# Performance work log

Measured on AMD Instinct MI355X. Metric: run time of the kernel, lower is better.

Reference implementation:

```python
import jax, jax.numpy as jnp
import numpy as np
import math

D, H, NQP, NKP = 512, 8, 4, 4
DH = D // H
OUT_DIM = D + H * NKP * 3  # 608


def setup_inputs() -> dict:
    key = jax.random.key(0)
    ks = jax.random.split(key, 12)
    B, L = 2, 1024
    s = jax.random.normal(ks[0], (B, L, D), dtype=jnp.float32)
    R = jax.random.normal(ks[1], (B, L, 3, 3), dtype=jnp.float32)
    tr = jax.random.normal(ks[2], (B, L, 3), dtype=jnp.float32)
    sc = 0.02
    Wq = jax.random.normal(ks[3], (D, D), dtype=jnp.float32) * sc
    Wk = jax.random.normal(ks[4], (D, D), dtype=jnp.float32) * sc
    Wv = jax.random.normal(ks[5], (D, D), dtype=jnp.float32) * sc
    Wqp = jax.random.normal(ks[6], (D, H * NQP * 3), dtype=jnp.float32) * sc
    Wkp = jax.random.normal(ks[7], (D, H * NKP * 3), dtype=jnp.float32) * sc
    Wvp = jax.random.normal(ks[8], (D, H * NKP * 3), dtype=jnp.float32) * sc
    Wo = jax.random.normal(ks[9], (OUT_DIM, D), dtype=jnp.float32) * sc
    bo = jnp.zeros((D,), dtype=jnp.float32)
    gamma = jnp.ones((D,), dtype=jnp.float32)
    beta = jnp.zeros((D,), dtype=jnp.float32)
    w_C = jnp.full((H,), math.log(20.0), dtype=jnp.float32)
    return dict(s=s, R=R, tr=tr, Wq=Wq, Wk=Wk, Wv=Wv, Wqp=Wqp, Wkp=Wkp,
                Wvp=Wvp, Wo=Wo, bo=bo, gamma=gamma, beta=beta, w_C=w_C)


def _layernorm(x, gamma, beta, eps=1e-5):
    mu = jnp.mean(x, axis=-1, keepdims=True)
    var = jnp.var(x, axis=-1, keepdims=True)
    return (x - mu) * jax.lax.rsqrt(var + eps) * gamma + beta


def reference(s, R, tr, Wq, Wk, Wv, Wqp, Wkp, Wvp, Wo, bo, gamma, beta, w_C):
    B, L, _ = s.shape
    # scalar q/k/v: (B, L, H, dh)
    Q = (s @ Wq).reshape(B, L, H, DH)
    K = (s @ Wk).reshape(B, L, H, DH)
    V = (s @ Wv).reshape(B, L, H, DH)
    a_s = jnp.einsum('bihd,bjhd->bhij', Q, K) / math.sqrt(DH)
    # local points: (B, L, H, P, 3)
    Qp = (s @ Wqp).reshape(B, L, H, NQP, 3)
    Kp = (s @ Wkp).reshape(B, L, H, NKP, 3)
    Vp = (s @ Wvp).reshape(B, L, H, NKP, 3)
    tr_e = tr[:, :, None, None, :]
    to_global = lambda p: jnp.einsum('blxy,blhpy->blhpx', R, p) + tr_e
    Qp_g, Kp_g, Vp_g = to_global(Qp), to_global(Kp), to_global(Vp)
    # (B, H, L, P, 3)
    qh = jnp.transpose(Qp_g, (0, 2, 1, 3, 4))
    kh = jnp.transpose(Kp_g, (0, 2, 1, 3, 4))
    diff = qh[:, :, :, None] - kh[:, :, None]          # (B,H,L,L,P,3)
    sq_dist = jnp.sum(diff * diff, axis=(-2, -1))      # (B,H,L,L)
    wc = jax.nn.softplus(w_C)[None, :, None, None]
    attn = jax.nn.softmax(a_s - 0.5 * wc * sq_dist, axis=-1)
    out_s = jnp.einsum('bhij,bjhd->bihd', attn, V).reshape(B, L, D)
    Vp_agg = jnp.einsum('bhij,bjhpc->bihpc', attn, Vp_g)  # (B,L,H,P,3)
    # global -> local: R^T (p - tr)
    Vp_local = jnp.einsum('blyx,blhpy->blhpx', R, Vp_agg - tr_e)
    out_p = Vp_local.reshape(B, L, H * NKP * 3)
    out = jnp.concatenate([out_s, out_p], axis=-1) @ Wo + bo
    return _layernorm(s + out, gamma, beta)
```

## Files before the change

### kernel.cpp

```cpp
#include <hip/hip_runtime.h>
#include <hip/hip_fp16.h>
#include <math.h>

typedef _Float16 f16;
typedef _Float16 f16x8 __attribute__((ext_vector_type(8)));
typedef _Float16 f16x4v __attribute__((ext_vector_type(4)));
typedef float f32x4 __attribute__((ext_vector_type(4)));

#define BATCH   2
#define LSEQ    1024
#define BLTOT   2048
#define DMODEL  512
#define NHEAD   8
#define PDIM    1824
#define AW      96
#define ODIM    608
#define NSPLIT  2

__global__ __launch_bounds__(256)
void prep_kernel(const float* __restrict__ s,
                 const float* __restrict__ Wq, const float* __restrict__ Wk,
                 const float* __restrict__ Wv, const float* __restrict__ Wqp,
                 const float* __restrict__ Wkp, const float* __restrict__ Wvp,
                 const float* __restrict__ Wo,
                 f16* __restrict__ sH, f16* __restrict__ WallT, f16* __restrict__ WoT)
{
    const int blk = blockIdx.x;
    const int t = threadIdx.x;
    __shared__ float tile[32][33];

    if (blk < 1024) {
        const int i = blk * 256 + t;
        float4 v = ((const float4*)s)[i];
        f16x4v o = { (f16)v.x, (f16)v.y, (f16)v.z, (f16)v.w };
        ((f16x4v*)sH)[i] = o;
        return;
    }
    if (blk < 1936) {
        const int idx = blk - 1024;
        const int n0 = (idx % 57) * 32, k0 = (idx / 57) * 32;
        const float* src; int ld, nc0;
        if      (n0 < 512)  { src = Wq;  ld = 512; nc0 = n0; }
        else if (n0 < 1024) { src = Wk;  ld = 512; nc0 = n0 - 512; }
        else if (n0 < 1536) { src = Wv;  ld = 512; nc0 = n0 - 1024; }
        else if (n0 < 1632) { src = Wqp; ld = 96;  nc0 = n0 - 1536; }
        else if (n0 < 1728) { src = Wkp; ld = 96;  nc0 = n0 - 1632; }
        else                { src = Wvp; ld = 96;  nc0 = n0 - 1728; }
#pragma unroll
        for (int i = 0; i < 4; ++i) {
            const int idx2 = t + i * 256;
            const int kl = idx2 >> 5, nl = idx2 & 31;
            tile[kl][nl] = src[(long long)(k0 + kl) * ld + nc0 + nl];
        }
        __syncthreads();
#pragma unroll
        for (int i = 0; i < 4; ++i) {
            const int idx2 = t + i * 256;
            const int nl = idx2 >> 5, kl = idx2 & 31;
            WallT[(long long)(n0 + nl) * 512 + k0 + kl] = (f16)tile[kl][nl];
        }
        return;
    }
    {
        const int idx = blk - 1936;
        const int n0 = (idx % 16) * 32, k0 = (idx / 16) * 32;
#pragma unroll
        for (int i = 0; i < 4; ++i) {
            const int idx2 = t + i * 256;
            const int kl = idx2 >> 5, nl = idx2 & 31;
            tile[kl][nl] = Wo[(long long)(k0 + kl) * 512 + n0 + nl];
        }
        __syncthreads();
#pragma unroll
        for (int i = 0; i < 4; ++i) {
            const int idx2 = t + i * 256;
            const int nl = idx2 >> 5, kl = idx2 & 31;
            WoT[(long long)(n0 + nl) * 608 + k0 + kl] = (f16)tile[kl][nl];
        }
    }
}

template<int BN, bool OUT16>
__global__ __launch_bounds__(256)
void gemm2_kernel(const f16* __restrict__ A, const f16* __restrict__ Bt,
                  void* __restrict__ Cout, int K, int ldc)
{
    constexpr int BCH = (BN * 4 + 255) / 256;
    __shared__ f16 As[2][64][40];
    __shared__ f16 Bs[2][BN][40];
    const int t = threadIdx.x;
    const int w = t >> 6, lane = t & 63, l15 = lane & 15, lhi = lane >> 4;
    const int row0 = blockIdx.y * 64, col0 = blockIdx.x * BN;
    const int ar = t >> 2, ac = t & 3;

    f32x4 acc[BN / 16];
#pragma unroll
    for (int n = 0; n < BN / 16; ++n) acc[n] = (f32x4){0.f, 0.f, 0.f, 0.f};

    const int nsteps = K >> 5;

    f16x8 aR;
    f16x8 bR[BCH];
    aR = *(const f16x8*)&A[(long long)(row0 + ar) * K + ac * 8];
#pragma unroll
    for (int i = 0; i < BCH; ++i) {
        const int cid = t + i * 256;
        if (cid < BN * 4) {
            const int br = cid >> 2, bc = cid & 3;
            bR[i] = *(const f16x8*)&Bt[(long long)(col0 + br) * K + bc * 8];
        }
    }
    *(f16x8*)&As[0][ar][ac * 8] = aR;
#pragma unroll
    for (int i = 0; i < BCH; ++i) {
        const int cid = t + i * 256;
        if (cid < BN * 4) *(f16x8*)&Bs[0][cid >> 2][(cid & 3) * 8] = bR[i];
    }
    __syncthreads();

    for (int st = 0; st < nsteps; ++st) {
        const int cur = st & 1;
        if (st + 1 < nsteps) {
            const int k0 = (st + 1) << 5;
            aR = *(const f16x8*)&A[(long long)(row0 + ar) * K + k0 + ac * 8];
#pragma unroll
            for (int i = 0; i < BCH; ++i) {
                const int cid = t + i * 256;
                if (cid < BN * 4) {
                    const int br = cid >> 2, bc = cid & 3;
                    bR[i] = *(const f16x8*)&Bt[(long long)(col0 + br) * K + k0 + bc * 8];
                }
            }
        }
        f16x8 af = *(const f16x8*)&As[cur][w * 16 + l15][lhi * 8];
        f16x8 bf[BN / 16];
#pragma unroll
        for (int n = 0; n < BN / 16; ++n)
            bf[n] = *(const f16x8*)&Bs[cur][n * 16 + l15][lhi * 8];
#pragma unroll
        for (int n = 0; n < BN / 16; ++n)
            acc[n] = __builtin_amdgcn_mfma_f32_16x16x32_f16(af, bf[n], acc[n], 0, 0, 0);
        if (st + 1 < nsteps) {
            *(f16x8*)&As[cur ^ 1][ar][ac * 8] = aR;
#pragma unroll
            for (int i = 0; i < BCH; ++i) {
                const int cid = t + i * 256;
                if (cid < BN * 4) *(f16x8*)&Bs[cur ^ 1][cid >> 2][(cid & 3) * 8] = bR[i];
            }
        }
        __syncthreads();
    }

    const int row = row0 + w * 16 + lhi * 4;
#pragma unroll
    for (int n = 0; n < BN / 16; ++n) {
        const int col = col0 + n * 16 + l15;
#pragma unroll
        for (int r = 0; r < 4; ++r) {
            if (OUT16) ((f16*)Cout)[(long long)(row + r) * ldc + col] = (f16)acc[n][r];
            else       ((float*)Cout)[(long long)(row + r) * ldc + col] = acc[n][r];
        }
    }
}

__global__ __launch_bounds__(256)
void build_aug2_kernel(const f16* __restrict__ P, const float* __restrict__ Rm,
                       const float* __restrict__ tr, const float* __restrict__ wC,
                       f16* __restrict__ QA, f16* __restrict__ KA,
                       f16* __restrict__ VCT, float* __restrict__ KOFF)
{
    const int l0 = blockIdx.x * 64;
    const int bh = blockIdx.y;
    const int b = bh >> 3, h = bh & 7;
    const int t = threadIdx.x;

    __shared__ float Rl[64][9];
    __shared__ float trl[64][3];
    __shared__ f16 gq[64][12];
    __shared__ f16 gk[64][12];
    __shared__ float k2[64][4];
    __shared__ f16 Vt[96][72];
    __shared__ float wcs;

    const long long blbase = (long long)b * LSEQ + l0;

    for (int i = t; i < 64 * 9; i += 256) Rl[i / 9][i % 9] = Rm[blbase * 9 + i];
    for (int i = t; i < 64 * 3; i += 256) trl[i / 3][i % 3] = tr[blbase * 3 + i];
    if (t == 0) { float x = wC[h]; wcs = log1pf(expf(x)); }
    __syncthreads();
    const float wc = wcs;

    for (int i = t; i < 768; i += 256) {
        const int l = i / 12, pp = i - l * 12;
        const int proj = pp >> 2, p = pp & 3;
        const f16* src = P + (blbase + l) * PDIM + 1536 + proj * 96 + h * 12 + p * 3;
        const float x = (float)src[0], y = (float)src[1], z = (float)src[2];
        const float gx = Rl[l][0]*x + Rl[l][1]*y + Rl[l][2]*z + trl[l][0];
        const float gy = Rl[l][3]*x + Rl[l][4]*y + Rl[l][5]*z + trl[l][1];
        const float gz = Rl[l][6]*x + Rl[l][7]*y + Rl[l][8]*z + trl[l][2];
        if (proj == 0) {
            gq[l][p * 3 + 0] = (f16)(wc * gx);
            gq[l][p * 3 + 1] = (f16)(wc * gy);
            gq[l][p * 3 + 2] = (f16)(wc * gz);
        } else if (proj == 1) {
            gk[l][p * 3 + 0] = (f16)gx;
            gk[l][p * 3 + 1] = (f16)gy;
            gk[l][p * 3 + 2] = (f16)gz;
            k2[l][p] = gx * gx + gy * gy + gz * gz;
        } else {
            Vt[64 + p * 3 + 0][l] = (f16)gx;
            Vt[64 + p * 3 + 1][l] = (f16)gy;
            Vt[64 + p * 3 + 2][l] = (f16)gz;
        }
    }
    for (int i = t; i < 512; i += 256) {
        const int l = i >> 3, ch = i & 7;
        f16x8 v = *(const f16x8*)&P[(blbase + l) * PDIM + 1024 + h * 64 + ch * 8];
#pragma unroll
        for (int j = 0; j < 8; ++j) Vt[ch * 8 + j][l] = v[j];
    }
    for (int i = t; i < 180; i += 256) {
        const int r = 76 + i / 9, ch = i % 9;
        *(f16x8*)&Vt[r][ch * 8] = (f16x8){0,0,0,0,0,0,0,0};
    }
    __syncthreads();

    if (t < 64)
        KOFF[(long long)bh * LSEQ + l0 + t] =
            0.5f * wc * (k2[t][0] + k2[t][1] + k2[t][2] + k2[t][3]);

    for (int i = t; i < 768; i += 256) {
        const int l = i / 12, ch = i - l * 12;
        const long long prow = (blbase + l) * PDIM;
        const long long orow = ((long long)bh * LSEQ + l0 + l) * AW;
        f16x8 q, k;
        if (ch < 8) {
            f16x8 qv = *(const f16x8*)&P[prow + h * 64 + ch * 8];
            f16x8 kv = *(const f16x8*)&P[prow + 512 + h * 64 + ch * 8];
            q = qv * (f16)0.125f;
            k = kv;
        } else if (ch == 8) {
#pragma unroll
            for (int j = 0; j < 8; ++j) { q[j] = gq[l][j]; k[j] = gk[l][j]; }
        } else if (ch == 9) {
#pragma unroll
            for (int j = 0; j < 8; ++j) {
                q[j] = (j < 4) ? gq[l][8 + j] : (f16)0.f;
                k[j] = (j < 4) ? gk[l][8 + j] : (f16)0.f;
            }
        } else {
            q = (f16x8){0,0,0,0,0,0,0,0};
            k = (f16x8){0,0,0,0,0,0,0,0};
        }
        *(f16x8*)&QA[orow + ch * 8] = q;
        *(f16x8*)&KA[orow + ch * 8] = k;
    }
    for (int i = t; i < 768; i += 256) {
        const int c = i >> 3, lg = i & 7;
        *(f16x8*)&VCT[((long long)bh * AW + c) * LSEQ + l0 + lg * 8] =
            *(const f16x8*)&Vt[c][lg * 8];
    }
}

__global__ __launch_bounds__(256, 2)
void attn_kernel(const f16* __restrict__ QA, const f16* __restrict__ KA,
                 const f16* __restrict__ VCT, const float* __restrict__ KOFF,
                 f16* __restrict__ OCp, float2* __restrict__ ML)
{
    const int bh = blockIdx.y;
    const int q0 = blockIdx.x * 64;
    const int z  = blockIdx.z;
    const int t = threadIdx.x;
    const int w = t >> 6, lane = t & 63, l15 = lane & 15, lhi = lane >> 4;

    __shared__ f16 Ks[128][104];
    __shared__ f16 Vs[96][136];
    __shared__ f16 Ps[64][136];

    const f16* qbase = QA + ((long long)bh * LSEQ + q0 + w * 16 + l15) * AW;
    f16x8 qf[3];
#pragma unroll
    for (int ks = 0; ks < 3; ++ks)
        qf[ks] = *(const f16x8*)(qbase + ks * 32 + lhi * 8);

    f32x4 Oacc[6];
#pragma unroll
    for (int nv = 0; nv < 6; ++nv) Oacc[nv] = (f32x4){0.f, 0.f, 0.f, 0.f};
    float M[4], L[4];
#pragma unroll
    for (int r = 0; r < 4; ++r) { M[r] = -1e30f; L[r] = 0.f; }

    const f16* kgbase = KA + (long long)bh * LSEQ * AW;
    const f16* vgbase = VCT + (long long)bh * AW * LSEQ;
    const float* koffb = KOFF + (long long)bh * LSEQ;

    const int kvbeg = z * (LSEQ / NSPLIT);
    const int kvend = kvbeg + LSEQ / NSPLIT;

#pragma unroll
    for (int i = 0; i < 6; ++i) {
        const int cid = t + i * 256;
        const int r = cid / 12, c = cid - r * 12;
        *(f16x8*)&Ks[r][c * 8] = *(const f16x8*)(kgbase + (long long)(kvbeg + r) * AW + c * 8);
    }
#pragma unroll
    for (int i = 0; i < 6; ++i) {
        const int cid = t + i * 256;
        const int r = cid >> 4, c = cid & 15;
        *(f16x8*)&Vs[r][c * 8] = *(const f16x8*)(vgbase + (long long)r * LSEQ + kvbeg + c * 8);
    }
    __syncthreads();

    for (int kv0 = kvbeg; kv0 < kvend; kv0 += 128) {
        const bool more = (kv0 + 128 < kvend);
        f16x8 kpre[6], vpre[6];
        if (more) {
#pragma unroll
            for (int i = 0; i < 6; ++i) {
                const int cid = t + i * 256;
                const int r = cid / 12, c = cid - r * 12;
                kpre[i] = *(const f16x8*)(kgbase + (long long)(kv0 + 128 + r) * AW + c * 8);
            }
#pragma unroll
            for (int i = 0; i < 6; ++i) {
                const int cid = t + i * 256;
                const int r = cid >> 4, c = cid & 15;
                vpre[i] = *(const f16x8*)(vgbase + (long long)r * LSEQ + kv0 + 128 + c * 8);
            }
        }

        f32x4 sc[8];
#pragma unroll
        for (int n = 0; n < 8; ++n) sc[n] = (f32x4){0.f, 0.f, 0.f, 0.f};
        __builtin_amdgcn_s_setprio(1);
#pragma unroll
        for (int n = 0; n < 8; ++n)
#pragma unroll
            for (int ks = 0; ks < 3; ++ks) {
                f16x8 kb = *(const f16x8*)&Ks[n * 16 + l15][ks * 32 + lhi * 8];
                sc[n] = __builtin_amdgcn_mfma_f32_16x16x32_f16(qf[ks], kb, sc[n], 0, 0, 0);
            }
        __builtin_amdgcn_s_setprio(0);
#pragma unroll
        for (int n = 0; n < 8; ++n) {
            const float ko = koffb[kv0 + n * 16 + l15];
#pragma unroll
            for (int r = 0; r < 4; ++r) sc[n][r] -= ko;
        }
        float sscale[4];
#pragma unroll
        for (int r = 0; r < 4; ++r) {
            float mr = sc[0][r];
#pragma unroll
            for (int n = 1; n < 8; ++n) mr = fmaxf(mr, sc[n][r]);
#pragma unroll
            for (int off = 1; off < 16; off <<= 1) mr = fmaxf(mr, __shfl_xor(mr, off));
            const float nm = fmaxf(M[r], mr);
            sscale[r] = __expf(M[r] - nm);
            M[r] = nm;
        }
        float rsum[4] = {0.f, 0.f, 0.f, 0.f};
#pragma unroll
        for (int n = 0; n < 8; ++n)
#pragma unroll
            for (int r = 0; r < 4; ++r) {
                const float p = __expf(sc[n][r] - M[r]);
                sc[n][r] = p;
                rsum[r] += p;
            }
#pragma unroll
        for (int r = 0; r < 4; ++r) {
            float s = rsum[r];
#pragma unroll
            for (int off = 1; off < 16; off <<= 1) s += __shfl_xor(s, off);
            L[r] = L[r] * sscale[r] + s;
        }
#pragma unroll
        for (int nv = 0; nv < 6; ++nv)
#pragma unroll
            for (int r = 0; r < 4; ++r) Oacc[nv][r] *= sscale[r];

#pragma unroll
        for (int n = 0; n < 8; ++n)
#pragma unroll
            for (int r = 0; r < 4; ++r)
                Ps[w * 16 + lhi * 4 + r][n * 16 + l15] = (f16)sc[n][r];

        f16x8 pa[4];
#pragma unroll
        for (int ks = 0; ks < 4; ++ks)
            pa[ks] = *(const f16x8*)&Ps[w * 16 + l15][ks * 32 + lhi * 8];
        __builtin_amdgcn_s_setprio(1);
#pragma unroll
        for (int nv = 0; nv < 6; ++nv)
#pragma unroll
            for (int ks = 0; ks < 4; ++ks) {
                f16x8 vb = *(const f16x8*)&Vs[nv * 16 + l15][ks * 32 + lhi * 8];
                Oacc[nv] = __builtin_amdgcn_mfma_f32_16x16x32_f16(pa[ks], vb, Oacc[nv], 0, 0, 0);
            }
        __builtin_amdgcn_s_setprio(0);
        __syncthreads();

        if (more) {
#pragma unroll
            for (int i = 0; i < 6; ++i) {
                const int cid = t + i * 256;
                const int r = cid / 12, c = cid - r * 12;
                *(f16x8*)&Ks[r][c * 8] = kpre[i];
            }
#pragma unroll
            for (int i = 0; i < 6; ++i) {
                const int cid = t + i * 256;
                const int r = cid >> 4, c = cid & 15;
                *(f16x8*)&Vs[r][c * 8] = vpre[i];
            }
        }
        __syncthreads();
    }

    f16* obase = OCp + (((long long)(z * 16 + bh) * LSEQ) + q0 + w * 16 + lhi * 4) * AW;
#pragma unroll
    for (int nv = 0; nv < 6; ++nv)
#pragma unroll
        for (int r = 0; r < 4; ++r)
            obase[r * AW + nv * 16 + l15] = (f16)Oacc[nv][r];
    if (l15 == 0) {
#pragma unroll
        for (int r = 0; r < 4; ++r)
            ML[(long long)(z * 16 + bh) * LSEQ + q0 + w * 16 + lhi * 4 + r] =
                make_float2(M[r], L[r]);
    }
}

__global__ __launch_bounds__(256)
void combine_concat_kernel(const f16* __restrict__ OCp, const float2* __restrict__ ML,
                           const float* __restrict__ Rm, const float* __restrict__ tr,
                           f16* __restrict__ CC)
{
    const int bl = blockIdx.x;
    const int b = bl >> 10, l = bl & 1023;
    const int t = threadIdx.x;

    __shared__ float w1[8], w2[8];
    __shared__ float o[8][AW];
    __shared__ float Rloc[9], trloc[3];
    if (t < 9) Rloc[t] = Rm[(long long)bl * 9 + t];
    if (t < 3) trloc[t] = tr[(long long)bl * 3 + t];
    if (t < 8) {
        const int bh = b * 8 + t;
        const float2 m1 = ML[(long long)bh * LSEQ + l];
        const float2 m2 = ML[(long long)(16 + bh) * LSEQ + l];
        const float mm = fmaxf(m1.x, m2.x);
        const float e1 = __expf(m1.x - mm), e2 = __expf(m2.x - mm);
        const float inv = 1.0f / (m1.y * e1 + m2.y * e2);
        w1[t] = e1 * inv; w2[t] = e2 * inv;
    }
    __syncthreads();
    for (int idx = t; idx < 8 * AW; idx += 256) {
        const int h = idx / AW, c = idx - h * AW;
        const f16* p1 = OCp + ((long long)(b * 8 + h) * LSEQ + l) * AW;
        const f16* p2 = OCp + ((long long)(16 + b * 8 + h) * LSEQ + l) * AW;
        o[h][c] = (float)p1[c] * w1[h] + (float)p2[c] * w2[h];
    }
    __syncthreads();

    f16* crow = CC + (long long)bl * ODIM;
    for (int c = t; c < DMODEL; c += 256) crow[c] = (f16)o[c >> 6][c & 63];
    if (t < 32) {
        const int h = t >> 2, p = t & 3;
        const float x = o[h][64 + p * 3 + 0] - trloc[0];
        const float y = o[h][64 + p * 3 + 1] - trloc[1];
        const float z = o[h][64 + p * 3 + 2] - trloc[2];
        crow[512 + h * 12 + p * 3 + 0] = (f16)(Rloc[0]*x + Rloc[3]*y + Rloc[6]*z);
        crow[512 + h * 12 + p * 3 + 1] = (f16)(Rloc[1]*x + Rloc[4]*y + Rloc[7]*z);
        crow[512 + h * 12 + p * 3 + 2] = (f16)(Rloc[2]*x + Rloc[5]*y + Rloc[8]*z);
    }
}

__global__ __launch_bounds__(256)
void residual_ln_kernel(const float* __restrict__ s, const float* __restrict__ Y,
                        const float* __restrict__ bo, const float* __restrict__ gamma,
                        const float* __restrict__ beta, float* __restrict__ out)
{
    const int bl = blockIdx.x;
    const int t = threadIdx.x;
    const float* srow = s + (long long)bl * DMODEL;
    const float* yrow = Y + (long long)bl * DMODEL;

    const float v0 = srow[t]       + yrow[t]       + bo[t];
    const float v1 = srow[t + 256] + yrow[t + 256] + bo[t + 256];

    float sum = v0 + v1, sq = v0 * v0 + v1 * v1;
#pragma unroll
    for (int o = 32; o > 0; o >>= 1) {
        sum += __shfl_xor(sum, o);
        sq  += __shfl_xor(sq,  o);
    }
    __shared__ float rs[4], rq[4];
    const int wid = t >> 6, lane = t & 63;
    if (lane == 0) { rs[wid] = sum; rq[wid] = sq; }
    __syncthreads();
    sum = rs[0] + rs[1] + rs[2] + rs[3];
    sq  = rq[0] + rq[1] + rq[2] + rq[3];

    const float mu  = sum * (1.0f / DMODEL);
    const float var = sq * (1.0f / DMODEL) - mu * mu;
    const float inv = rsqrtf(var + 1e-5f);

    out[(long long)bl * DMODEL + t]       = (v0 - mu) * inv * gamma[t]       + beta[t];
    out[(long long)bl * DMODEL + t + 256] = (v1 - mu) * inv * gamma[t + 256] + beta[t + 256];
}

extern "C" void kernel_launch(void* const* d_in, const int* in_sizes, int n_in,
                              void* d_out, int out_size, void* d_ws, size_t ws_size,
                              hipStream_t stream)
{
    const float* s    = (const float*)d_in[0];
    const float* R    = (const float*)d_in[1];
    const float* tr   = (const float*)d_in[2];
    const float* Wq   = (const float*)d_in[3];
    const float* Wk   = (const float*)d_in[4];
    const float* Wv   = (const float*)d_in[5];
    const float* Wqp  = (const float*)d_in[6];
    const float* Wkp  = (const float*)d_in[7];
    const float* Wvp  = (const float*)d_in[8];
    const float* Wo   = (const float*)d_in[9];
    const float* bo   = (const float*)d_in[10];
    const float* gam  = (const float*)d_in[11];
    const float* bet  = (const float*)d_in[12];
    const float* wC   = (const float*)d_in[13];
    float* out = (float*)d_out;

    f16* sH    = (f16*)d_ws;
    f16* WallT = sH + 1048576;
    f16* WoT   = WallT + 933888;
    f16* P     = WoT + 311296;
    f16* QA    = P + 3735552;
    f16* KA    = QA + 1572864;
    f16* VCT   = KA + 1572864;
    float* KOFF = (float*)(VCT + 1572864);
    f16* OCp    = (f16*)(KOFF + 16384);
    float2* ML  = (float2*)(OCp + 3145728);
    f16* CC     = (f16*)(ML + 32768);
    float* Y    = (float*)(CC + 1245184);

    const dim3 blk(256);

    prep_kernel<<<dim3(2240), blk, 0, stream>>>(s, Wq, Wk, Wv, Wqp, Wkp, Wvp, Wo,
                                                sH, WallT, WoT);

    gemm2_kernel<96, true><<<dim3(19, 32), blk, 0, stream>>>(sH, WallT, P, 512, 1824);

    build_aug2_kernel<<<dim3(16, 16), blk, 0, stream>>>(P, R, tr, wC, QA, KA, VCT, KOFF);

    attn_kernel<<<dim3(16, 16, NSPLIT), blk, 0, stream>>>(QA, KA, VCT, KOFF, OCp, ML);

    combine_concat_kernel<<<dim3(BLTOT), blk, 0, stream>>>(OCp, ML, R, tr, CC);

    gemm2_kernel<64, false><<<dim3(8, 32), blk, 0, stream>>>(CC, WoT, Y, 608, 512);

    residual_ln_kernel<<<dim3(BLTOT), blk, 0, stream>>>(s, Y, bo, gam, bet, out);
}
```

Measured before the change: 72.90 us.

## Fuse projection epilogue into GEMM and split-combine into output GEMM

The QKV/point projection GEMM now writes scaled Q, K, transposed V and rigid-transformed point features straight into the attention input layouts from its epilogue. This removes the intermediate P buffer and the separate build kernel. The split-softmax combine and the global-to-local point rotation move into the A-operand load path of the output-projection GEMM, which removes the CC buffer and the combine kernel. The cost is heavier epilogues with scattered narrow stores, recomputed combine weights for each column tile, and extra global reads of OCp per N-tile.

Result: slower. 88.06 us (+20.8%).

```diff
diff --git a/kernel.cpp b/kernel.cpp
--- a/kernel.cpp
+++ b/kernel.cpp
@@ -12,10 +12,9 @@
 #define BLTOT   2048
 #define DMODEL  512
 #define NHEAD   8
-#define PDIM    1824
 #define AW      96
-#define ODIM    608
 #define NSPLIT  2
+#define OCPSTR  1572864
 
 __global__ __launch_bounds__(256)
 void prep_kernel(const float* __restrict__ s,
@@ -80,185 +79,169 @@
     }
 }
 
-template<int BN, bool OUT16>
+struct SmG { f16 As[2][64][40]; f16 Bs[2][96][40]; };
+struct SmE { float pts[64][96]; float Rl[64][9]; float trl[64][3]; };
+
 __global__ __launch_bounds__(256)
-void gemm2_kernel(const f16* __restrict__ A, const f16* __restrict__ Bt,
-                  void* __restrict__ Cout, int K, int ldc)
+void proj_fused_kernel(const f16* __restrict__ A, const f16* __restrict__ Bt,
+                       const float* __restrict__ Rm, const float* __restrict__ tr,
+                       const float* __restrict__ wC,
+                       f16* __restrict__ QA, f16* __restrict__ KA,
+                       f16* __restrict__ VCT, float* __restrict__ KOFF)
 {
-    constexpr int BCH = (BN * 4 + 255) / 256;
-    __shared__ f16 As[2][64][40];
-    __shared__ f16 Bs[2][BN][40];
+    __shared__ union { SmG g; SmE e; } sm;
     const int t = threadIdx.x;
     const int w = t >> 6, lane = t & 63, l15 = lane & 15, lhi = lane >> 4;
-    const int row0 = blockIdx.y * 64, col0 = blockIdx.x * BN;
+    const int row0 = blockIdx.y * 64, col0 = blockIdx.x * 96;
     const int ar = t >> 2, ac = t & 3;
-
-    f32x4 acc[BN / 16];
-#pragma unroll
-    for (int n = 0; n < BN / 16; ++n) acc[n] = (f32x4){0.f, 0.f, 0.f, 0.f};
-
-    const int nsteps = K >> 5;
-
-    f16x8 aR;
-    f16x8 bR[BCH];
+    const int K = 512;
+
+    f32x4 acc[6];
+#pragma unroll
+    for (int n = 0; n < 6; ++n) acc[n] = (f32x4){0.f, 0.f, 0.f, 0.f};
+
+    f16x8 aR, bR[2];
     aR = *(const f16x8*)&A[(long long)(row0 + ar) * K + ac * 8];
 #pragma unroll
-    for (int i = 0; i < BCH; ++i) {
+    for (int i = 0; i < 2; ++i) {
         const int cid = t + i * 256;
-        if (cid < BN * 4) {
+        if (cid < 384) {
             const int br = cid >> 2, bc = cid & 3;
             bR[i] = *(const f16x8*)&Bt[(long long)(col0 + br) * K + bc * 8];
         }
     }
-    *(f16x8*)&As[0][ar][ac * 8] = aR;
-#pragma unroll
-    for (int i = 0; i < BCH; ++i) {
+    *(f16x8*)&sm.g.As[0][ar][ac * 8] = aR;
+#pragma unroll
+    for (int i = 0; i < 2; ++i) {
         const int cid = t + i * 256;
-        if (cid < BN * 4) *(f16x8*)&Bs[0][cid >> 2][(cid & 3) * 8] = bR[i];
+        if (cid < 384) *(f16x8*)&sm.g.Bs[0][cid >> 2][(cid & 3) * 8] = bR[i];
     }
     __syncthreads();
 
-    for (int st = 0; st < nsteps; ++st) {
+    for (int st = 0; st < 16; ++st) {
         const int cur = st & 1;
-        if (st + 1 < nsteps) {
+        if (st + 1 < 16) {
             const int k0 = (st + 1) << 5;
             aR = *(const f16x8*)&A[(long long)(row0 + ar) * K + k0 + ac * 8];
 #pragma unroll
-            for (int i = 0; i < BCH; ++i) {
+            for (int i = 0; i < 2; ++i) {
                 const int cid = t + i * 256;
-                if (cid < BN * 4) {
+                if (cid < 384) {
                     const int br = cid >> 2, bc = cid & 3;
                     bR[i] = *(const f16x8*)&Bt[(long long)(col0 + br) * K + k0 + bc * 8];
                 }
             }
         }
-        f16x8 af = *(const f16x8*)&As[cur][w * 16 + l15][lhi * 8];
-        f16x8 bf[BN / 16];
-#pragma unroll
-        for (int n = 0; n < BN / 16; ++n)
-            bf[n] = *(const f16x8*)&Bs[cur][n * 16 + l15][lhi * 8];
-#pragma unroll
-        for (int n = 0; n < BN / 16; ++n)
+        f16x8 af = *(const f16x8*)&sm.g.As[cur][w * 16 + l15][lhi * 8];
+        f16x8 bf[6];
+#pragma unroll
+        for (int n = 0; n < 6; ++n)
+            bf[n] = *(const f16x8*)&sm.g.Bs[cur][n * 16 + l15][lhi * 8];
+#pragma unroll
+        for (int n = 0; n < 6; ++n)
             acc[n] = __builtin_amdgcn_mfma_f32_16x16x32_f16(af, bf[n], acc[n], 0, 0, 0);
-        if (st + 1 < nsteps) {
-            *(f16x8*)&As[cur ^ 1][ar][ac * 8] = aR;
-#pragma unroll
-            for (int i = 0; i < BCH; ++i) {
+        if (st + 1 < 16) {
+            *(f16x8*)&sm.g.As[cur ^ 1][ar][ac * 8] = aR;
+#pragma unroll
+            for (int i = 0; i < 2; ++i) {
                 const int cid = t + i * 256;
-                if (cid < BN * 4) *(f16x8*)&Bs[cur ^ 1][cid >> 2][(cid & 3) * 8] = bR[i];
+                if (cid < 384) *(f16x8*)&sm.g.Bs[cur ^ 1][cid >> 2][(cid & 3) * 8] = bR[i];
             }
         }
         __syncthreads();
     }
 
-    const int row = row0 + w * 16 + lhi * 4;
-#pragma unroll
-    for (int n = 0; n < BN / 16; ++n) {
-        const int col = col0 + n * 16 + l15;
-#pragma unroll
-        for (int r = 0; r < 4; ++r) {
-            if (OUT16) ((f16*)Cout)[(long long)(row + r) * ldc + col] = (f16)acc[n][r];
-            else       ((float*)Cout)[(long long)(row + r) * ldc + col] = acc[n][r];
-        }
-    }
-}
-
-__global__ __launch_bounds__(256)
-void build_aug2_kernel(const f16* __restrict__ P, const float* __restrict__ Rm,
-                       const float* __restrict__ tr, const float* __restrict__ wC,
-                       f16* __restrict__ QA, f16* __restrict__ KA,
-                       f16* __restrict__ VCT, float* __restrict__ KOFF)
-{
-    const int l0 = blockIdx.x * 64;
-    const int bh = blockIdx.y;
-    const int b = bh >> 3, h = bh & 7;
-    const int t = threadIdx.x;
-
-    __shared__ float Rl[64][9];
-    __shared__ float trl[64][3];
-    __shared__ f16 gq[64][12];
-    __shared__ f16 gk[64][12];
-    __shared__ float k2[64][4];
-    __shared__ f16 Vt[96][72];
-    __shared__ float wcs;
-
-    const long long blbase = (long long)b * LSEQ + l0;
-
-    for (int i = t; i < 64 * 9; i += 256) Rl[i / 9][i % 9] = Rm[blbase * 9 + i];
-    for (int i = t; i < 64 * 3; i += 256) trl[i / 3][i % 3] = tr[blbase * 3 + i];
-    if (t == 0) { float x = wC[h]; wcs = log1pf(expf(x)); }
+    const int xt = blockIdx.x;
+    const int b = row0 >> 10;
+
+    if (xt < 16) {
+        const int row = row0 + w * 16 + lhi * 4;
+        const int l = row & 1023;
+#pragma unroll
+        for (int n = 0; n < 6; ++n) {
+            const int gc = col0 + n * 16 + l15;
+            if (gc < 512) {
+                const int h = gc >> 6, ch = gc & 63;
+                f16* dst = &QA[((long long)(b * 8 + h) * 1024 + l) * AW + ch];
+#pragma unroll
+                for (int r = 0; r < 4; ++r) dst[r * AW] = (f16)(acc[n][r] * 0.125f);
+            } else if (gc < 1024) {
+                const int h = (gc - 512) >> 6, ch = gc & 63;
+                f16* dst = &KA[((long long)(b * 8 + h) * 1024 + l) * AW + ch];
+#pragma unroll
+                for (int r = 0; r < 4; ++r) dst[r * AW] = (f16)acc[n][r];
+            } else {
+                const int lc = gc - 1024, h = lc >> 6, ch = lc & 63;
+                f16x4v v = { (f16)acc[n][0], (f16)acc[n][1], (f16)acc[n][2], (f16)acc[n][3] };
+                *(f16x4v*)&VCT[((long long)(b * 8 + h) * AW + ch) * 1024 + l] = v;
+            }
+        }
+        return;
+    }
+
+#pragma unroll
+    for (int n = 0; n < 6; ++n) {
+        const int c = n * 16 + l15;
+        const int rr = w * 16 + lhi * 4;
+#pragma unroll
+        for (int r = 0; r < 4; ++r) sm.e.pts[rr + r][c] = acc[n][r];
+    }
+    for (int i = t; i < 64 * 9; i += 256) sm.e.Rl[i / 9][i % 9] = Rm[(long long)row0 * 9 + i];
+    for (int i = t; i < 64 * 3; i += 256) sm.e.trl[i / 3][i % 3] = tr[(long long)row0 * 3 + i];
     __syncthreads();
-    const float wc = wcs;
-
-    for (int i = t; i < 768; i += 256) {
-        const int l = i / 12, pp = i - l * 12;
-        const int proj = pp >> 2, p = pp & 3;
-        const f16* src = P + (blbase + l) * PDIM + 1536 + proj * 96 + h * 12 + p * 3;
-        const float x = (float)src[0], y = (float)src[1], z = (float)src[2];
-        const float gx = Rl[l][0]*x + Rl[l][1]*y + Rl[l][2]*z + trl[l][0];
-        const float gy = Rl[l][3]*x + Rl[l][4]*y + Rl[l][5]*z + trl[l][1];
-        const float gz = Rl[l][6]*x + Rl[l][7]*y + Rl[l][8]*z + trl[l][2];
+
+    const int proj = xt - 16;
+    const f16x8 zero8 = (f16x8){0,0,0,0,0,0,0,0};
+
+    for (int idx = t; idx < 512; idx += 256) {
+        const int i = idx >> 3, h = idx & 7;
+        const int l = (row0 + i) & 1023;
+        const long long rowoff = ((long long)(b * 8 + h) * 1024 + l) * AW;
+        const float wcx = wC[h];
+        const float wc = log1pf(expf(wcx));
+        float s2 = 0.f;
+#pragma unroll
+        for (int p = 0; p < 4; ++p) {
+            const float vx = sm.e.pts[i][h * 12 + p * 3 + 0];
+            const float vy = sm.e.pts[i][h * 12 + p * 3 + 1];
+            const float vz = sm.e.pts[i][h * 12 + p * 3 + 2];
+            const float gx = sm.e.Rl[i][0]*vx + sm.e.Rl[i][1]*vy + sm.e.Rl[i][2]*vz + sm.e.trl[i][0];
+            const float gy = sm.e.Rl[i][3]*vx + sm.e.Rl[i][4]*vy + sm.e.Rl[i][5]*vz + sm.e.trl[i][1];
+            const float gz = sm.e.Rl[i][6]*vx + sm.e.Rl[i][7]*vy + sm.e.Rl[i][8]*vz + sm.e.trl[i][2];
+            if (proj == 0) {
+                QA[rowoff + 64 + p * 3 + 0] = (f16)(wc * gx);
+                QA[rowoff + 64 + p * 3 + 1] = (f16)(wc * gy);
+                QA[rowoff + 64 + p * 3 + 2] = (f16)(wc * gz);
+            } else if (proj == 1) {
+                KA[rowoff + 64 + p * 3 + 0] = (f16)gx;
+                KA[rowoff + 64 + p * 3 + 1] = (f16)gy;
+                KA[rowoff + 64 + p * 3 + 2] = (f16)gz;
+                s2 += gx * gx + gy * gy + gz * gz;
+            } else {
+                VCT[((long long)(b * 8 + h) * AW + 64 + p * 3 + 0) * 1024 + l] = (f16)gx;
+                VCT[((long long)(b * 8 + h) * AW + 64 + p * 3 + 1) * 1024 + l] = (f16)gy;
+                VCT[((long long)(b * 8 + h) * AW + 64 + p * 3 + 2) * 1024 + l] = (f16)gz;
+            }
+        }
         if (proj == 0) {
-            gq[l][p * 3 + 0] = (f16)(wc * gx);
-            gq[l][p * 3 + 1] = (f16)(wc * gy);
-            gq[l][p * 3 + 2] = (f16)(wc * gz);
+            f16* dst = &QA[rowoff];
+            *(f16x4v*)&dst[76] = (f16x4v){0,0,0,0};
+            *(f16x8*)&dst[80] = zero8;
+            *(f16x8*)&dst[88] = zero8;
         } else if (proj == 1) {
-            gk[l][p * 3 + 0] = (f16)gx;
-            gk[l][p * 3 + 1] = (f16)gy;
-            gk[l][p * 3 + 2] = (f16)gz;
-            k2[l][p] = gx * gx + gy * gy + gz * gz;
-        } else {
-            Vt[64 + p * 3 + 0][l] = (f16)gx;
-            Vt[64 + p * 3 + 1][l] = (f16)gy;
-            Vt[64 + p * 3 + 2][l] = (f16)gz;
-        }
-    }
-    for (int i = t; i < 512; i += 256) {
-        const int l = i >> 3, ch = i & 7;
-        f16x8 v = *(const f16x8*)&P[(blbase + l) * PDIM + 1024 + h * 64 + ch * 8];
-#pragma unroll
-        for (int j = 0; j < 8; ++j) Vt[ch * 8 + j][l] = v[j];
-    }
-    for (int i = t; i < 180; i += 256) {
-        const int r = 76 + i / 9, ch = i % 9;
-        *(f16x8*)&Vt[r][ch * 8] = (f16x8){0,0,0,0,0,0,0,0};
-    }
-    __syncthreads();
-
-    if (t < 64)
-        KOFF[(long long)bh * LSEQ + l0 + t] =
-            0.5f * wc * (k2[t][0] + k2[t][1] + k2[t][2] + k2[t][3]);
-
-    for (int i = t; i < 768; i += 256) {
-        const int l = i / 12, ch = i - l * 12;
-        const long long prow = (blbase + l) * PDIM;
-        const long long orow = ((long long)bh * LSEQ + l0 + l) * AW;
-        f16x8 q, k;
-        if (ch < 8) {
-            f16x8 qv = *(const f16x8*)&P[prow + h * 64 + ch * 8];
-            f16x8 kv = *(const f16x8*)&P[prow + 512 + h * 64 + ch * 8];
-            q = qv * (f16)0.125f;
-            k = kv;
-        } else if (ch == 8) {
-#pragma unroll
-            for (int j = 0; j < 8; ++j) { q[j] = gq[l][j]; k[j] = gk[l][j]; }
-        } else if (ch == 9) {
-#pragma unroll
-            for (int j = 0; j < 8; ++j) {
-                q[j] = (j < 4) ? gq[l][8 + j] : (f16)0.f;
-                k[j] = (j < 4) ? gk[l][8 + j] : (f16)0.f;
-            }
-        } else {
-            q = (f16x8){0,0,0,0,0,0,0,0};
-            k = (f16x8){0,0,0,0,0,0,0,0};
-        }
-        *(f16x8*)&QA[orow + ch * 8] = q;
-        *(f16x8*)&KA[orow + ch * 8] = k;
-    }
-    for (int i = t; i < 768; i += 256) {
-        const int c = i >> 3, lg = i & 7;
-        *(f16x8*)&VCT[((long long)bh * AW + c) * LSEQ + l0 + lg * 8] =
-            *(const f16x8*)&Vt[c][lg * 8];
+            KOFF[(long long)(b * 8 + h) * 1024 + l] = 0.5f * wc * s2;
+            f16* dst = &KA[rowoff];
+            *(f16x4v*)&dst[76] = (f16x4v){0,0,0,0};
+            *(f16x8*)&dst[80] = zero8;
+            *(f16x8*)&dst[88] = zero8;
+        }
+    }
+    if (proj == 2) {
+        for (int idx = t; idx < 8 * 20 * 8; idx += 256) {
+            const int h = idx / 160, rem = idx - h * 160;
+            const int r = 76 + rem / 8, lg = rem & 7;
+            *(f16x8*)&VCT[((long long)(b * 8 + h) * AW + r) * 1024 + (row0 & 1023) + lg * 8] = zero8;
+        }
     }
 }
 
@@ -433,47 +416,122 @@
 }
 
 __global__ __launch_bounds__(256)
-void combine_concat_kernel(const f16* __restrict__ OCp, const float2* __restrict__ ML,
-                           const float* __restrict__ Rm, const float* __restrict__ tr,
-                           f16* __restrict__ CC)
+void gemm_comb_kernel(const f16* __restrict__ OCp, const float2* __restrict__ ML,
+                      const float* __restrict__ Rm, const float* __restrict__ tr,
+                      const f16* __restrict__ WoT, float* __restrict__ Y)
 {
-    const int bl = blockIdx.x;
-    const int b = bl >> 10, l = bl & 1023;
+    __shared__ f16 As[2][64][40];
+    __shared__ f16 Bs[2][64][40];
+    __shared__ f16 ccp[64][96];
+    __shared__ float w1s[64][8], w2s[64][8];
+    __shared__ float Rl[64][9], trl[64][3];
+
     const int t = threadIdx.x;
-
-    __shared__ float w1[8], w2[8];
-    __shared__ float o[8][AW];
-    __shared__ float Rloc[9], trloc[3];
-    if (t < 9) Rloc[t] = Rm[(long long)bl * 9 + t];
-    if (t < 3) trloc[t] = tr[(long long)bl * 3 + t];
-    if (t < 8) {
-        const int bh = b * 8 + t;
-        const float2 m1 = ML[(long long)bh * LSEQ + l];
-        const float2 m2 = ML[(long long)(16 + bh) * LSEQ + l];
+    const int w = t >> 6, lane = t & 63, l15 = lane & 15, lhi = lane >> 4;
+    const int row0 = blockIdx.y * 64, col0 = blockIdx.x * 64;
+    const int b = row0 >> 10;
+    const int ai = t >> 2, as = t & 3;
+
+    for (int i = t; i < 64 * 9; i += 256) Rl[i / 9][i % 9] = Rm[(long long)row0 * 9 + i];
+    for (int i = t; i < 64 * 3; i += 256) trl[i / 3][i % 3] = tr[(long long)row0 * 3 + i];
+    for (int idx = t; idx < 512; idx += 256) {
+        const int i = idx >> 3, h = idx & 7;
+        const int l = (row0 + i) & 1023;
+        const int bh = b * 8 + h;
+        const float2 m1 = ML[(long long)bh * 1024 + l];
+        const float2 m2 = ML[(long long)(16 + bh) * 1024 + l];
         const float mm = fmaxf(m1.x, m2.x);
         const float e1 = __expf(m1.x - mm), e2 = __expf(m2.x - mm);
         const float inv = 1.0f / (m1.y * e1 + m2.y * e2);
-        w1[t] = e1 * inv; w2[t] = e2 * inv;
+        w1s[i][h] = e1 * inv; w2s[i][h] = e2 * inv;
     }
     __syncthreads();
-    for (int idx = t; idx < 8 * AW; idx += 256) {
-        const int h = idx / AW, c = idx - h * AW;
-        const f16* p1 = OCp + ((long long)(b * 8 + h) * LSEQ + l) * AW;
-        const f16* p2 = OCp + ((long long)(16 + b * 8 + h) * LSEQ + l) * AW;
-        o[h][c] = (float)p1[c] * w1[h] + (float)p2[c] * w2[h];
+
+    for (int idx = t; idx < 2048; idx += 256) {
+        const int i = idx >> 5, hp = idx & 31, h = hp >> 2, p = hp & 3;
+        const int l = (row0 + i) & 1023;
+        const long long base = ((long long)(b * 8 + h) * 1024 + l) * AW + 64 + p * 3;
+        const float w1 = w1s[i][h], w2 = w2s[i][h];
+        float o[3];
+#pragma unroll
+        for (int c = 0; c < 3; ++c)
+            o[c] = w1 * (float)OCp[base + c] + w2 * (float)OCp[OCPSTR + base + c] - trl[i][c];
+        ccp[i][h * 12 + p * 3 + 0] = (f16)(Rl[i][0]*o[0] + Rl[i][3]*o[1] + Rl[i][6]*o[2]);
+        ccp[i][h * 12 + p * 3 + 1] = (f16)(Rl[i][1]*o[0] + Rl[i][4]*o[1] + Rl[i][7]*o[2]);
+        ccp[i][h * 12 + p * 3 + 2] = (f16)(Rl[i][2]*o[0] + Rl[i][5]*o[1] + Rl[i][8]*o[2]);
     }
     __syncthreads();
 
-    f16* crow = CC + (long long)bl * ODIM;
-    for (int c = t; c < DMODEL; c += 256) crow[c] = (f16)o[c >> 6][c & 63];
-    if (t < 32) {
-        const int h = t >> 2, p = t & 3;
-        const float x = o[h][64 + p * 3 + 0] - trloc[0];
-        const float y = o[h][64 + p * 3 + 1] - trloc[1];
-        const float z = o[h][64 + p * 3 + 2] - trloc[2];
-        crow[512 + h * 12 + p * 3 + 0] = (f16)(Rloc[0]*x + Rloc[3]*y + Rloc[6]*z);
-        crow[512 + h * 12 + p * 3 + 1] = (f16)(Rloc[1]*x + Rloc[4]*y + Rloc[7]*z);
-        crow[512 + h * 12 + p * 3 + 2] = (f16)(Rloc[2]*x + Rloc[5]*y + Rloc[8]*z);
+    f32x4 acc[4];
+#pragma unroll
+    for (int n = 0; n < 4; ++n) acc[n] = (f32x4){0.f, 0.f, 0.f, 0.f};
+
+    f16x8 a1R, a2R, bR;
+    const int l_ai = (row0 + ai) & 1023;
+
+    {
+        const int col = as * 8;
+        const int h = col >> 6, ch = col & 63;
+        const long long base = ((long long)(b * 8 + h) * 1024 + l_ai) * AW + ch;
+        f16x8 p1 = *(const f16x8*)&OCp[base];
+        f16x8 p2 = *(const f16x8*)&OCp[OCPSTR + base];
+        const float w1 = w1s[ai][h], w2 = w2s[ai][h];
+        f16x8 v;
+#pragma unroll
+        for (int j = 0; j < 8; ++j) v[j] = (f16)(w1 * (float)p1[j] + w2 * (float)p2[j]);
+        *(f16x8*)&As[0][ai][as * 8] = v;
+        bR = *(const f16x8*)&WoT[(long long)(col0 + ai) * 608 + as * 8];
+        *(f16x8*)&Bs[0][ai][as * 8] = bR;
+    }
+    __syncthreads();
+
+    for (int st = 0; st < 19; ++st) {
+        const int cur = st & 1;
+        const int nk0 = (st + 1) << 5;
+        const bool more = (st + 1 < 19);
+        bool nIsC = false;
+        if (more) {
+            const int col = nk0 + as * 8;
+            if (col < 512) {
+                const int h = col >> 6, ch = col & 63;
+                const long long base = ((long long)(b * 8 + h) * 1024 + l_ai) * AW + ch;
+                a1R = *(const f16x8*)&OCp[base];
+                a2R = *(const f16x8*)&OCp[OCPSTR + base];
+            } else nIsC = true;
+            bR = *(const f16x8*)&WoT[(long long)(col0 + ai) * 608 + nk0 + as * 8];
+        }
+        f16x8 af = *(const f16x8*)&As[cur][w * 16 + l15][lhi * 8];
+        f16x8 bf[4];
+#pragma unroll
+        for (int n = 0; n < 4; ++n)
+            bf[n] = *(const f16x8*)&Bs[cur][n * 16 + l15][lhi * 8];
+#pragma unroll
+        for (int n = 0; n < 4; ++n)
+            acc[n] = __builtin_amdgcn_mfma_f32_16x16x32_f16(af, bf[n], acc[n], 0, 0, 0);
+        if (more) {
+            f16x8 v;
+            if (!nIsC) {
+                const int col = nk0 + as * 8;
+                const int h = col >> 6;
+                const float w1 = w1s[ai][h], w2 = w2s[ai][h];
+#pragma unroll
+                for (int j = 0; j < 8; ++j) v[j] = (f16)(w1 * (float)a1R[j] + w2 * (float)a2R[j]);
+            } else {
+                v = *(const f16x8*)&ccp[ai][nk0 + as * 8 - 512];
+            }
+            *(f16x8*)&As[cur ^ 1][ai][as * 8] = v;
+            *(f16x8*)&Bs[cur ^ 1][ai][as * 8] = bR;
+        }
+        __syncthreads();
+    }
+
+    const int row = row0 + w * 16 + lhi * 4;
+#pragma unroll
+    for (int n = 0; n < 4; ++n) {
+        const int col = col0 + n * 16 + l15;
+#pragma unroll
+        for (int r = 0; r < 4; ++r)
+            Y[(long long)(row + r) * 512 + col] = acc[n][r];
     }
 }
 
@@ -534,30 +592,25 @@
     f16* sH    = (f16*)d_ws;
     f16* WallT = sH + 1048576;
     f16* WoT   = WallT + 933888;
-    f16* P     = WoT + 311296;
-    f16* QA    = P + 3735552;
+    f16* QA    = WoT + 311296;
     f16* KA    = QA + 1572864;
     f16* VCT   = KA + 1572864;
     float* KOFF = (float*)(VCT + 1572864);
     f16* OCp    = (f16*)(KOFF + 16384);
     float2* ML  = (float2*)(OCp + 3145728);
-    f16* CC     = (f16*)(ML + 32768);
-    float* Y    = (float*)(CC + 1245184);
+    float* Y    = (float*)(ML + 32768);
 
     const dim3 blk(256);
 
     prep_kernel<<<dim3(2240), blk, 0, stream>>>(s, Wq, Wk, Wv, Wqp, Wkp, Wvp, Wo,
                                                 sH, WallT, WoT);
 
-    gemm2_kernel<96, true><<<dim3(19, 32), blk, 0, stream>>>(sH, WallT, P, 512, 1824);
-
-    build_aug2_kernel<<<dim3(16, 16), blk, 0, stream>>>(P, R, tr, wC, QA, KA, VCT, KOFF);
+    proj_fused_kernel<<<dim3(19, 32), blk, 0, stream>>>(sH, WallT, R, tr, wC,
+                                                        QA, KA, VCT, KOFF);
 
     attn_kernel<<<dim3(16, 16, NSPLIT), blk, 0, stream>>>(QA, KA, VCT, KOFF, OCp, ML);
 
-    combine_concat_kernel<<<dim3(BLTOT), blk, 0, stream>>>(OCp, ML, R, tr, CC);
-
-    gemm2_kernel<64, false><<<dim3(8, 32), blk, 0, stream>>>(CC, WoT, Y, 608, 512);
+    gemm_comb_kernel<<<dim3(8, 32), blk, 0, stream>>>(OCp, ML, R, tr, WoT, Y);
 
     residual_ln_kernel<<<dim3(BLTOT), blk, 0, stream>>>(s, Y, bo, gam, bet, out);
 }
```
